# Performance work log

Measured on AMD Instinct MI355X. Metric: run time of the kernel, lower is better.

Reference implementation:

```python
import jax, jax.numpy as jnp
import numpy as np

B, S, D, H, DM = 2, 2048, 1024, 16, 4
HD = D // H  # head_dim = 64
EPS = 1e-5


def setup_inputs() -> dict:
    key = jax.random.key(0)
    ks = jax.random.split(key, 8)
    s = 0.02
    return {
        "x": jax.random.normal(ks[0], (B, S, D), jnp.float32),
        "wq": jax.random.normal(ks[1], (D, D), jnp.float32) * s,
        "wk": jax.random.normal(ks[2], (D, D), jnp.float32) * s,
        "wv": jax.random.normal(ks[3], (D, D), jnp.float32) * s,
        "wo": jax.random.normal(ks[4], (D, D), jnp.float32) * s,
        "bo": jnp.zeros((D,), jnp.float32),
        "ln1_scale": jnp.ones((D,), jnp.float32),
        "ln1_shift": jnp.zeros((D,), jnp.float32),
        "ln2_scale": jnp.ones((D,), jnp.float32),
        "ln2_shift": jnp.zeros((D,), jnp.float32),
        "w1": jax.random.normal(ks[5], (DM * D, D), jnp.float32) * s,
        "b1": jnp.zeros((DM * D,), jnp.float32),
        "w2": jax.random.normal(ks[6], (D, DM * D), jnp.float32) * s,
        "b2": jnp.zeros((D,), jnp.float32),
    }


def _layernorm(x, scale, shift):
    mean = jnp.mean(x, axis=-1, keepdims=True)
    var = jnp.var(x, axis=-1, keepdims=True)  # unbiased=False
    return scale * (x - mean) * jax.lax.rsqrt(var + EPS) + shift


def _attn(x, wq, wk, wv, wo, bo):
    b, n, d = x.shape
    # torch Linear: y = x @ W.T
    q = (x @ wq.T).reshape(b, n, H, HD).transpose(0, 2, 1, 3)  # [b,h,n,hd]
    k = (x @ wk.T).reshape(b, n, H, HD).transpose(0, 2, 1, 3)
    v = (x @ wv.T).reshape(b, n, H, HD).transpose(0, 2, 1, 3)
    scores = jnp.einsum("bhqd,bhkd->bhqk", q, k)
    causal = jnp.tril(jnp.ones((n, n), bool))
    scores = jnp.where(causal, scores, -jnp.inf)
    w = jax.nn.softmax(scores / np.sqrt(HD).astype(np.float32), axis=-1)
    ctx = jnp.einsum("bhqk,bhkd->bhqd", w, v)
    ctx = ctx.transpose(0, 2, 1, 3).reshape(b, n, d)
    return ctx @ wo.T + bo


def reference(x, wq, wk, wv, wo, bo, ln1_scale, ln1_shift, ln2_scale, ln2_shift, w1, b1, w2, b2):
    h = x + _attn(_layernorm(x, ln1_scale, ln1_shift), wq, wk, wv, wo, bo)
    y = _layernorm(h, ln2_scale, ln2_shift)
    y = jax.nn.relu(y @ w1.T + b1) @ w2.T + b2
    return h + y
```

## Files before the change

kernel.cpp:

```cpp
#include <hip/hip_runtime.h>
#include <hip/hip_bf16.h>

#define DEV __device__ __forceinline__

typedef __attribute__((ext_vector_type(8))) short bf8;
typedef __attribute__((ext_vector_type(4))) float f4;
typedef __attribute__((ext_vector_type(16))) float f16x;

#define GLOAD_LDS(gp, lp) \
  __builtin_amdgcn_global_load_lds( \
      (const __attribute__((address_space(1))) void*)(gp), \
      (__attribute__((address_space(3))) void*)(lp), 16, 0, 0)

DEV unsigned short f2bf(float f) {
  union { __hip_bfloat16 h; unsigned short u; } c;
  c.h = __float2bfloat16(f);
  return c.u;
}
DEV unsigned int pk2(float a, float b) {
  union { __hip_bfloat162 h; unsigned int u; } c;
  c.h = __hip_bfloat162(__float2bfloat16(a), __float2bfloat16(b));
  return c.u;
}

DEV int2 swz_tile(int ob, int nxt, int nyt) {
  const int nb = nxt * nyt;
  const int cpx = nb >> 3;
  const int W = (ob & 7) * cpx + (ob >> 3);
  const int scw = 4 * nyt;
  const int sc = W / scw, rem = W - sc * scw;
  return make_int2(rem >> 2, sc * 4 + (rem & 3));
}

template<bool BIAS, bool RELU, bool OUTBF, bool WRVT>
__global__ __launch_bounds__(512, 2) void gemm_bt256(
    const unsigned short* __restrict__ A, const unsigned short* __restrict__ B,
    const float* __restrict__ bias, void* __restrict__ Cout,
    int M, int N, int K, int ldc, unsigned short* __restrict__ vtout, int nyt)
{
  __shared__ unsigned short Sl[2][2][256 * 64];
  const int t = threadIdx.x;
  const int w = t >> 6, l = t & 63;
  const int wr = w >> 2, wc = w & 3;
  int2 tt = swz_tile((int)blockIdx.x, N >> 8, nyt);
  const int m0 = tt.x * 256, n0 = tt.y * 256;

  const int srow = w * 32 + (l >> 3);
  const int scol = 8 * ((l & 7) ^ (l >> 3));
  const unsigned short* Ab = A + (size_t)(m0 + srow) * K + scol;
  const unsigned short* Bb = B + (size_t)(n0 + srow) * K + scol;
  const int sdst = w * 2048 + l * 8;

  auto STAGE = [&](int slot, int kt) {
#pragma unroll
    for (int i = 0; i < 4; ++i) {
      GLOAD_LDS(Ab + (size_t)i * 8 * K + kt * 64, &Sl[slot][0][sdst + i * 512]);
      GLOAD_LDS(Bb + (size_t)i * 8 * K + kt * 64, &Sl[slot][1][sdst + i * 512]);
    }
  };

  const f4 fz = {0.f, 0.f, 0.f, 0.f};
  f4 acc[8][4];
#pragma unroll
  for (int i = 0; i < 8; ++i)
#pragma unroll
    for (int j = 0; j < 4; ++j) acc[i][j] = fz;

  const int NT = K >> 6;
  STAGE(0, 0);
  __syncthreads();

  for (int T = 0; T < NT; ++T) {
    if (T + 1 < NT) STAGE((T + 1) & 1, T + 1);
    const int sl = T & 1;
#pragma unroll
    for (int ks = 0; ks < 2; ++ks) {
      const int cb = (ks * 64 + ((l >> 4) * 16)) ^ ((l & 7) << 4);
      bf8 af[8], bg[4];
#pragma unroll
      for (int m = 0; m < 8; ++m)
        af[m] = *(const bf8*)((const char*)&Sl[sl][0][(wr * 128 + m * 16 + (l & 15)) * 64] + cb);
#pragma unroll
      for (int n = 0; n < 4; ++n)
        bg[n] = *(const bf8*)((const char*)&Sl[sl][1][(wc * 64 + n * 16 + (l & 15)) * 64] + cb);
      __builtin_amdgcn_s_setprio(1);
#pragma unroll
      for (int m = 0; m < 8; ++m)
#pragma unroll
        for (int n = 0; n < 4; ++n)
          acc[m][n] = __builtin_amdgcn_mfma_f32_16x16x32_bf16(af[m], bg[n], acc[m][n], 0, 0, 0);
      __builtin_amdgcn_s_setprio(0);
    }
    __syncthreads();
  }

#pragma unroll
  for (int n = 0; n < 4; ++n) {
    const int col = n0 + wc * 64 + n * 16 + (l & 15);
    float bv = 0.f;
    if (BIAS) bv = bias[col];
    const bool isv = WRVT && (col >= 2048);
    const int hh = (col - 2048) >> 6, dd = (col - 2048) & 63;
#pragma unroll
    for (int m = 0; m < 8; ++m) {
#pragma unroll
      for (int r = 0; r < 4; ++r) {
        const int row = m0 + wr * 128 + m * 16 + ((l >> 4) * 4) + r;
        float v = acc[m][n][r] + bv;
        if (RELU) v = fmaxf(v, 0.f);
        if (WRVT && isv) {
          const int bb = row >> 11, ss = row & 2047;
          vtout[((size_t)(bb * 16 + hh) * 64 + dd) * 2048 + ss] = f2bf(v);
        } else if (OUTBF) {
          ((unsigned short*)Cout)[(size_t)row * ldc + col] = f2bf(v);
        } else {
          ((float*)Cout)[(size_t)row * ldc + col] = v;
        }
      }
    }
  }
}

template<bool BIAS, bool RELU, bool RESID, bool OUTBF>
__global__ __launch_bounds__(256) void gemm_bt64(
    const unsigned short* __restrict__ A, const unsigned short* __restrict__ B,
    const float* __restrict__ bias, const float* __restrict__ resid,
    void* __restrict__ Cout, int M, int N, int K, int ldc)
{
  __shared__ unsigned short Al[2][64 * 64];
  __shared__ unsigned short Bl[2][128 * 64];
  const int t = threadIdx.x;
  const int w = t >> 6, l = t & 63;
  const int wr = w >> 1, wc = w & 1;
  int2 tt = swz_tile((int)blockIdx.x, N >> 7, M >> 6);
  const int m0 = tt.x * 64, n0 = tt.y * 128;

  const int srow = t >> 3;
  const int scol = 8 * ((t & 7) ^ (srow & 7));
  const unsigned short* Ab = A + (size_t)(m0 + srow) * K + scol;
  const unsigned short* Bb = B + (size_t)(n0 + srow) * K + scol;
  const int sdst = srow * 64 + (t & 7) * 8;

  auto STAGE = [&](int slot, int k0) {
#pragma unroll
    for (int i = 0; i < 2; ++i)
      GLOAD_LDS(Ab + (size_t)(i * 32) * K + k0, &Al[slot][sdst + i * 32 * 64]);
#pragma unroll
    for (int i = 0; i < 4; ++i)
      GLOAD_LDS(Bb + (size_t)(i * 32) * K + k0, &Bl[slot][sdst + i * 32 * 64]);
  };

  const f4 fz = {0.f, 0.f, 0.f, 0.f};
  f4 acc[2][4];
#pragma unroll
  for (int i = 0; i < 2; ++i)
#pragma unroll
    for (int j = 0; j < 4; ++j) acc[i][j] = fz;

  const int NT = K >> 6;
  STAGE(0, 0);
  __syncthreads();

  for (int T = 0; T < NT; ++T) {
    if (T + 1 < NT) STAGE((T + 1) & 1, (T + 1) * 64);
    const int sl = T & 1;
#pragma unroll
    for (int ks = 0; ks < 2; ++ks) {
      const int cb = (ks * 64 + ((l >> 4) * 16)) ^ ((l & 7) << 4);
      bf8 af[2], bg[4];
#pragma unroll
      for (int am = 0; am < 2; ++am)
        af[am] = *(const bf8*)((const char*)&Al[sl][(wr * 32 + am * 16 + (l & 15)) * 64] + cb);
#pragma unroll
      for (int bn = 0; bn < 4; ++bn)
        bg[bn] = *(const bf8*)((const char*)&Bl[sl][(wc * 64 + bn * 16 + (l & 15)) * 64] + cb);
      __builtin_amdgcn_s_setprio(1);
#pragma unroll
      for (int am = 0; am < 2; ++am)
#pragma unroll
        for (int bn = 0; bn < 4; ++bn)
          acc[am][bn] = __builtin_amdgcn_mfma_f32_16x16x32_bf16(af[am], bg[bn], acc[am][bn], 0, 0, 0);
      __builtin_amdgcn_s_setprio(0);
    }
    __syncthreads();
  }

#pragma unroll
  for (int bn = 0; bn < 4; ++bn) {
    const int col = n0 + wc * 64 + bn * 16 + (l & 15);
    float bv = 0.f;
    if (BIAS) bv = bias[col];
#pragma unroll
    for (int am = 0; am < 2; ++am) {
#pragma unroll
      for (int r = 0; r < 4; ++r) {
        const int row = m0 + wr * 32 + am * 16 + ((l >> 4) * 4) + r;
        float v = acc[am][bn][r] + bv;
        if (RELU) v = fmaxf(v, 0.f);
        if (RESID) v += resid[(size_t)row * ldc + col];
        if (OUTBF) ((unsigned short*)Cout)[(size_t)row * ldc + col] = f2bf(v);
        else       ((float*)Cout)[(size_t)row * ldc + col] = v;
      }
    }
  }
}

__global__ __launch_bounds__(256, 4) void attn_kernel(
    const unsigned short* __restrict__ qk, const unsigned short* __restrict__ vt,
    unsigned short* __restrict__ ctx)
{
  __shared__ unsigned short SM[2][2][64 * 64];

  const int t = threadIdx.x;
  const int w = t >> 6, l = t & 63;
  const int p = w >> 1;
  const int hi = l >> 5, q = l & 31;
  const int bid = blockIdx.x;
  const int xcd = bid & 7, i = bid >> 3;
  const int g = i >> 5, c = i & 31;
  const int s = (g & 1) ? c : 31 - c;
  const int bh = xcd * 4 + g;
  const int b = bh >> 4, h = bh & 15;
  const int tile = 2 * s + (w & 1);
  const int q0w = tile * 32;
  const int h0 = (s + 2) >> 1;

  const unsigned short* qbase = qk + ((size_t)b * 2048) * 2048 + h * 64;
  const unsigned short* kbase = qbase + 1024;
  const unsigned short* vbase = vt + (size_t)bh * 64 * 2048;
  unsigned short* Kl = &SM[p][0][0];
  unsigned short* Vl = &SM[p][1][0];
  const int tp = t & 127;

  bf8 qf[4];
#pragma unroll
  for (int ksl = 0; ksl < 4; ++ksl)
    qf[ksl] = *(const bf8*)(qbase + (size_t)(q0w + q) * 2048 + ksl * 16 + hi * 8);

  f16x oacc[2];
#pragma unroll
  for (int dn = 0; dn < 2; ++dn)
#pragma unroll
    for (int i2 = 0; i2 < 16; ++i2) oacc[dn][i2] = 0.f;
  float m_ = -1e30f, l_ = 0.f;

  for (int it = 0; it < h0; ++it) {
    const int gi = p ? h0 + it : it;
    const bool act = gi <= s;
    __syncthreads();
    if (act) {
#pragma unroll
      for (int ss = 0; ss < 4; ++ss) {
        const int row = ss * 16 + (tp >> 3);
        const int cb = (tp & 7) * 16;
        const int sb = cb ^ ((row & 7) << 4);
        GLOAD_LDS(kbase + (size_t)(gi * 64 + row) * 2048 + (sb >> 1),
                  &Kl[row * 64 + (cb >> 1)]);
        GLOAD_LDS(vbase + (size_t)row * 2048 + gi * 64 + (sb >> 1),
                  &Vl[row * 64 + (cb >> 1)]);
      }
    }
    __syncthreads();
    if (act) {
      const int kb0 = gi * 64;

      f16x s0, s1;
#pragma unroll
      for (int i2 = 0; i2 < 16; ++i2) { s0[i2] = 0.f; s1[i2] = 0.f; }
      __builtin_amdgcn_s_setprio(1);
#pragma unroll
      for (int ksl = 0; ksl < 4; ++ksl) {
        const int cbq = (ksl * 16 + hi * 8) * 2;
        const int r0 = q, r1 = 32 + q;
        bf8 k0 = *(const bf8*)((const char*)&Kl[r0 * 64] + (cbq ^ ((r0 & 7) << 4)));
        bf8 k1 = *(const bf8*)((const char*)&Kl[r1 * 64] + (cbq ^ ((r1 & 7) << 4)));
        s0 = __builtin_amdgcn_mfma_f32_32x32x16_bf16(k0, qf[ksl], s0, 0, 0, 0);
        s1 = __builtin_amdgcn_mfma_f32_32x32x16_bf16(k1, qf[ksl], s1, 0, 0, 0);
      }
      __builtin_amdgcn_s_setprio(0);

      float pv[32];
      if (gi == s) {
#pragma unroll
        for (int i2 = 0; i2 < 16; ++i2) {
          const int key = kb0 + (i2 & 3) + 8 * (i2 >> 2) + 4 * hi;
          pv[i2]      = (key <= q0w + q)      ? s0[i2] : -1e30f;
          pv[16 + i2] = (key + 32 <= q0w + q) ? s1[i2] : -1e30f;
        }
      } else {
#pragma unroll
        for (int i2 = 0; i2 < 16; ++i2) { pv[i2] = s0[i2]; pv[16 + i2] = s1[i2]; }
      }

      float tm[16];
#pragma unroll
      for (int i2 = 0; i2 < 16; ++i2) tm[i2] = fmaxf(pv[i2], pv[16 + i2]);
#pragma unroll
      for (int st = 8; st >= 1; st >>= 1)
#pragma unroll
        for (int i2 = 0; i2 < 8; ++i2)
          if (i2 < st) tm[i2] = fmaxf(tm[i2], tm[i2 + st]);
      const float pmax = fmaxf(tm[0], __shfl_xor(tm[0], 32));
      if (__any(pmax > m_ + 11.54f)) {
        const float mn = fmaxf(m_, pmax);
        const float alpha = __builtin_amdgcn_exp2f(m_ - mn);
        m_ = mn;
        l_ *= alpha;
#pragma unroll
        for (int dn = 0; dn < 2; ++dn)
#pragma unroll
          for (int i2 = 0; i2 < 16; ++i2) oacc[dn][i2] *= alpha;
      }
#pragma unroll
      for (int i2 = 0; i2 < 32; ++i2) pv[i2] = __builtin_amdgcn_exp2f(pv[i2] - m_);
      float ts[16];
#pragma unroll
      for (int i2 = 0; i2 < 16; ++i2) ts[i2] = pv[i2] + pv[16 + i2];
#pragma unroll
      for (int st = 8; st >= 1; st >>= 1)
#pragma unroll
        for (int i2 = 0; i2 < 8; ++i2)
          if (i2 < st) ts[i2] += ts[i2 + st];
      l_ += ts[0] + __shfl_xor(ts[0], 32);

#pragma unroll
      for (int sg = 0; sg < 2; ++sg) {
        const float* pp = pv + sg * 16;
        unsigned int wds[8];
#pragma unroll
        for (int m = 0; m < 4; ++m) {
          wds[m * 2]     = pk2(pp[4 * m], pp[4 * m + 1]);
          wds[m * 2 + 1] = pk2(pp[4 * m + 2], pp[4 * m + 3]);
        }
#pragma unroll
        for (int kq = 0; kq < 2; ++kq) {
          unsigned int x0 = __shfl_xor((int)(hi ? wds[4 * kq]     : wds[4 * kq + 2]), 32);
          unsigned int x1 = __shfl_xor((int)(hi ? wds[4 * kq + 1] : wds[4 * kq + 3]), 32);
          union { unsigned int u[4]; bf8 v; } pu;
          pu.u[0] = hi ? x0 : wds[4 * kq];
          pu.u[1] = hi ? x1 : wds[4 * kq + 1];
          pu.u[2] = hi ? wds[4 * kq + 2] : x0;
          pu.u[3] = hi ? wds[4 * kq + 3] : x1;
          const bf8 pf = pu.v;
          __builtin_amdgcn_s_setprio(1);
#pragma unroll
          for (int dn = 0; dn < 2; ++dn) {
            const int row = dn * 32 + q;
            const int cb = ((sg * 32 + kq * 16 + hi * 8) * 2) ^ ((row & 7) << 4);
            bf8 vf = *(const bf8*)((const char*)&Vl[row * 64] + cb);
            oacc[dn] = __builtin_amdgcn_mfma_f32_32x32x16_bf16(vf, pf, oacc[dn], 0, 0, 0);
          }
          __builtin_amdgcn_s_setprio(0);
        }
      }
    }
  }

  __syncthreads();
  float* mb = (float*)&SM[0][0][0];
  if (p == 1) {
    float* base = mb + (w & 1) * 2176;
    base[l] = m_;
    base[64 + l] = l_;
#pragma unroll
    for (int dn = 0; dn < 2; ++dn)
#pragma unroll
      for (int i2 = 0; i2 < 16; ++i2)
        base[128 + (dn * 16 + i2) * 64 + l] = oacc[dn][i2];
  }
  __syncthreads();
  if (p == 0) {
    float* base = mb + (w & 1) * 2176;
    const float m2 = base[l], l2 = base[64 + l];
    const float mm = fmaxf(m_, m2);
    const float a0 = __builtin_amdgcn_exp2f(m_ - mm);
    const float a2 = __builtin_amdgcn_exp2f(m2 - mm);
    const float inv = 1.0f / (a0 * l_ + a2 * l2);
    unsigned short* crow = ctx + ((size_t)(b * 2048 + q0w + q)) * 1024 + h * 64;
#pragma unroll
    for (int dn = 0; dn < 2; ++dn)
#pragma unroll
      for (int m = 0; m < 4; ++m) {
        float o0 = a0 * oacc[dn][4 * m]     + a2 * base[128 + (dn * 16 + 4 * m) * 64 + l];
        float o1 = a0 * oacc[dn][4 * m + 1] + a2 * base[128 + (dn * 16 + 4 * m + 1) * 64 + l];
        float o2 = a0 * oacc[dn][4 * m + 2] + a2 * base[128 + (dn * 16 + 4 * m + 2) * 64 + l];
        float o3 = a0 * oacc[dn][4 * m + 3] + a2 * base[128 + (dn * 16 + 4 * m + 3) * 64 + l];
        const int d0 = dn * 32 + 8 * m + 4 * hi;
        *(unsigned int*)(crow + d0)     = pk2(o0 * inv, o1 * inv);
        *(unsigned int*)(crow + d0 + 2) = pk2(o2 * inv, o3 * inv);
      }
  }
}

__global__ __launch_bounds__(256) void ln_kernel(
    const float* __restrict__ x, const float* __restrict__ sc,
    const float* __restrict__ sh, unsigned short* __restrict__ out)
{
  const int row = blockIdx.x, t = threadIdx.x;
  float4 v = ((const float4*)x)[(size_t)row * 256 + t];
  float s = v.x + v.y + v.z + v.w;
  float q = v.x * v.x + v.y * v.y + v.z * v.z + v.w * v.w;
#pragma unroll
  for (int off = 1; off < 64; off <<= 1) {
    s += __shfl_xor(s, off);
    q += __shfl_xor(q, off);
  }
  __shared__ float red[8];
  const int w = t >> 6, l = t & 63;
  if (l == 0) { red[w] = s; red[4 + w] = q; }
  __syncthreads();
  s = red[0] + red[1] + red[2] + red[3];
  q = red[4] + red[5] + red[6] + red[7];
  const float mean = s * (1.0f / 1024.0f);
  const float var = q * (1.0f / 1024.0f) - mean * mean;
  const float rstd = rsqrtf(var + 1e-5f);
  float4 scv = ((const float4*)sc)[t];
  float4 shv = ((const float4*)sh)[t];
  uint2 p;
  p.x = pk2(scv.x * (v.x - mean) * rstd + shv.x, scv.y * (v.y - mean) * rstd + shv.y);
  p.y = pk2(scv.z * (v.z - mean) * rstd + shv.z, scv.w * (v.w - mean) * rstd + shv.w);
  ((uint2*)out)[(size_t)row * 256 + t] = p;
}

__global__ __launch_bounds__(256) void cvt_weights(
    const float* __restrict__ wq, const float* __restrict__ wk,
    const float* __restrict__ wv, const float* __restrict__ wo,
    const float* __restrict__ w1, const float* __restrict__ w2,
    unsigned short* __restrict__ dst)
{
  const int M1 = 1 << 20;
  const int n4 = (12 * M1) / 4;
  const int stride = gridDim.x * 256;
  for (int i4 = blockIdx.x * 256 + threadIdx.x; i4 < n4; i4 += stride) {
    const size_t i = (size_t)i4 * 4;
    const int mi = (int)(i >> 20);
    const float* src;
    size_t off;
    float sc = 1.0f;
    if (mi < 4) {
      src = mi == 0 ? wq : mi == 1 ? wk : mi == 2 ? wv : wo;
      off = i & (size_t)(M1 - 1);
      if (mi == 0) sc = 0.125f * 1.44269504088896f;
    } else if (mi < 8) {
      src = w1; off = i - (size_t)4 * M1;
    } else {
      src = w2; off = i - (size_t)8 * M1;
    }
    float4 v = *(const float4*)(src + off);
    uint2 pq;
    pq.x = pk2(v.x * sc, v.y * sc);
    pq.y = pk2(v.z * sc, v.w * sc);
    ((uint2*)dst)[i4] = pq;
  }
}

extern "C" void kernel_launch(void* const* d_in, const int* in_sizes, int n_in,
                              void* d_out, int out_size, void* d_ws, size_t ws_size,
                              hipStream_t stream)
{
  const float* x    = (const float*)d_in[0];
  const float* wq   = (const float*)d_in[1];
  const float* wk   = (const float*)d_in[2];
  const float* wv   = (const float*)d_in[3];
  const float* wo   = (const float*)d_in[4];
  const float* bo   = (const float*)d_in[5];
  const float* ln1s = (const float*)d_in[6];
  const float* ln1b = (const float*)d_in[7];
  const float* ln2s = (const float*)d_in[8];
  const float* ln2b = (const float*)d_in[9];
  const float* w1   = (const float*)d_in[10];
  const float* b1   = (const float*)d_in[11];
  const float* w2   = (const float*)d_in[12];
  const float* b2   = (const float*)d_in[13];
  float* out = (float*)d_out;

  const int M = 4096;

  unsigned short* ws   = (unsigned short*)d_ws;
  unsigned short* lnb  = ws;
  unsigned short* qkvw = lnb  + (size_t)4096 * 1024;
  unsigned short* wob  = qkvw + (size_t)3072 * 1024;
  unsigned short* w1b  = wob  + (size_t)1024 * 1024;
  unsigned short* w2b  = w1b  + (size_t)4096 * 1024;
  unsigned short* qkb  = w2b  + (size_t)4096 * 1024;
  unsigned short* vtb  = qkb  + (size_t)4096 * 2048;
  unsigned short* ctxb = vtb  + (size_t)32 * 64 * 2048;
  float* hf = (float*)(ctxb + (size_t)4096 * 1024);

  cvt_weights<<<2048, 256, 0, stream>>>(wq, wk, wv, wo, w1, w2, qkvw);

  ln_kernel<<<M, 256, 0, stream>>>(x, ln1s, ln1b, lnb);
  gemm_bt256<false, false, true, true><<<192, 512, 0, stream>>>(
      lnb, qkvw, nullptr, qkb, M, 3072, 1024, 2048, vtb, 16);
  attn_kernel<<<1024, 256, 0, stream>>>(qkb, vtb, ctxb);
  gemm_bt64<true, false, true, false><<<512, 256, 0, stream>>>(
      ctxb, wob, bo, x, hf, M, 1024, 1024, 1024);
  ln_kernel<<<M, 256, 0, stream>>>(hf, ln2s, ln2b, lnb);
  gemm_bt256<true, true, true, false><<<256, 512, 0, stream>>>(
      lnb, w1b, b1, qkb, M, 4096, 1024, 4096, nullptr, 16);
  gemm_bt64<true, false, true, false><<<512, 256, 0, stream>>>(
      qkb, w2b, b2, hf, out, M, 1024, 4096, 1024);
}
```

Baseline: 237.2 us.

## Replace 256x256 GEMM kernel with 128x128 tiles, BK=32, 256 threads

Replaces the 512-thread 256x256-tile GEMM with a 256-thread 128x128-tile variant that uses BK=32, a new LDS swizzle and a smaller accumulator set. It also adds an optional residual epilogue. The QKV and FFN1 launches move to 768 and 1024 blocks. This trades per-block data reuse and MFMA density for more blocks, better CU occupancy and less LDS per block, at the cost of more global traffic and more barriers per unit of work.

```diff
diff --git a/kernel.cpp b/kernel.cpp
--- a/kernel.cpp
+++ b/kernel.cpp
@@ -32,82 +32,82 @@
   return make_int2(rem >> 2, sc * 4 + (rem & 3));
 }
 
-template<bool BIAS, bool RELU, bool OUTBF, bool WRVT>
-__global__ __launch_bounds__(512, 2) void gemm_bt256(
+template<bool BIAS, bool RELU, bool RESID, bool OUTBF, bool WRVT>
+__global__ __launch_bounds__(256) void gemm_bt128(
     const unsigned short* __restrict__ A, const unsigned short* __restrict__ B,
-    const float* __restrict__ bias, void* __restrict__ Cout,
-    int M, int N, int K, int ldc, unsigned short* __restrict__ vtout, int nyt)
+    const float* __restrict__ bias, const float* __restrict__ resid,
+    void* __restrict__ Cout, int M, int N, int K, int ldc,
+    unsigned short* __restrict__ vtout, int nyt)
 {
-  __shared__ unsigned short Sl[2][2][256 * 64];
+  __shared__ unsigned short Al[2][128 * 32];
+  __shared__ unsigned short Bl[2][128 * 32];
   const int t = threadIdx.x;
   const int w = t >> 6, l = t & 63;
-  const int wr = w >> 2, wc = w & 3;
-  int2 tt = swz_tile((int)blockIdx.x, N >> 8, nyt);
-  const int m0 = tt.x * 256, n0 = tt.y * 256;
-
-  const int srow = w * 32 + (l >> 3);
-  const int scol = 8 * ((l & 7) ^ (l >> 3));
-  const unsigned short* Ab = A + (size_t)(m0 + srow) * K + scol;
-  const unsigned short* Bb = B + (size_t)(n0 + srow) * K + scol;
-  const int sdst = w * 2048 + l * 8;
-
-  auto STAGE = [&](int slot, int kt) {
-#pragma unroll
-    for (int i = 0; i < 4; ++i) {
-      GLOAD_LDS(Ab + (size_t)i * 8 * K + kt * 64, &Sl[slot][0][sdst + i * 512]);
-      GLOAD_LDS(Bb + (size_t)i * 8 * K + kt * 64, &Sl[slot][1][sdst + i * 512]);
+  const int wr = w >> 1, wc = w & 1;
+  int2 tt = swz_tile((int)blockIdx.x, N >> 7, nyt);
+  const int m0 = tt.x * 128, n0 = tt.y * 128;
+
+  const int srow = w * 16 + (l >> 2);
+  const int scsw = ((l & 3) * 8) ^ (((srow >> 1) & 3) << 3);
+  const unsigned short* Ab = A + (size_t)(m0 + srow) * K + scsw;
+  const unsigned short* Bb = B + (size_t)(n0 + srow) * K + scsw;
+  const int sdst = w * 512 + l * 8;
+
+  auto STAGE = [&](int slot, int k0) {
+#pragma unroll
+    for (int i = 0; i < 2; ++i) {
+      GLOAD_LDS(Ab + (size_t)i * 64 * K + k0, &Al[slot][sdst + i * 2048]);
+      GLOAD_LDS(Bb + (size_t)i * 64 * K + k0, &Bl[slot][sdst + i * 2048]);
     }
   };
 
   const f4 fz = {0.f, 0.f, 0.f, 0.f};
-  f4 acc[8][4];
-#pragma unroll
-  for (int i = 0; i < 8; ++i)
+  f4 acc[4][4];
+#pragma unroll
+  for (int i = 0; i < 4; ++i)
 #pragma unroll
     for (int j = 0; j < 4; ++j) acc[i][j] = fz;
 
-  const int NT = K >> 6;
+  const int NT = K >> 5;
   STAGE(0, 0);
   __syncthreads();
 
   for (int T = 0; T < NT; ++T) {
-    if (T + 1 < NT) STAGE((T + 1) & 1, T + 1);
+    if (T + 1 < NT) STAGE((T + 1) & 1, (T + 1) * 32);
     const int sl = T & 1;
-#pragma unroll
-    for (int ks = 0; ks < 2; ++ks) {
-      const int cb = (ks * 64 + ((l >> 4) * 16)) ^ ((l & 7) << 4);
-      bf8 af[8], bg[4];
-#pragma unroll
-      for (int m = 0; m < 8; ++m)
-        af[m] = *(const bf8*)((const char*)&Sl[sl][0][(wr * 128 + m * 16 + (l & 15)) * 64] + cb);
-#pragma unroll
-      for (int n = 0; n < 4; ++n)
-        bg[n] = *(const bf8*)((const char*)&Sl[sl][1][(wc * 64 + n * 16 + (l & 15)) * 64] + cb);
-      __builtin_amdgcn_s_setprio(1);
-#pragma unroll
-      for (int m = 0; m < 8; ++m)
-#pragma unroll
-        for (int n = 0; n < 4; ++n)
-          acc[m][n] = __builtin_amdgcn_mfma_f32_16x16x32_bf16(af[m], bg[n], acc[m][n], 0, 0, 0);
-      __builtin_amdgcn_s_setprio(0);
-    }
+    const int rdcol = ((l >> 4) * 8) ^ ((((l & 15) >> 1) & 3) << 3);
+    bf8 af[4], bg[4];
+#pragma unroll
+    for (int am = 0; am < 4; ++am)
+      af[am] = *(const bf8*)&Al[sl][(wr * 64 + am * 16 + (l & 15)) * 32 + rdcol];
+#pragma unroll
+    for (int bn = 0; bn < 4; ++bn)
+      bg[bn] = *(const bf8*)&Bl[sl][(wc * 64 + bn * 16 + (l & 15)) * 32 + rdcol];
+    __builtin_amdgcn_s_setprio(1);
+#pragma unroll
+    for (int am = 0; am < 4; ++am)
+#pragma unroll
+      for (int bn = 0; bn < 4; ++bn)
+        acc[am][bn] = __builtin_amdgcn_mfma_f32_16x16x32_bf16(af[am], bg[bn], acc[am][bn], 0, 0, 0);
+    __builtin_amdgcn_s_setprio(0);
     __syncthreads();
   }
 
 #pragma unroll
-  for (int n = 0; n < 4; ++n) {
-    const int col = n0 + wc * 64 + n * 16 + (l & 15);
+  for (int bn = 0; bn < 4; ++bn) {
+    const int col = n0 + wc * 64 + bn * 16 + (l & 15);
     float bv = 0.f;
     if (BIAS) bv = bias[col];
     const bool isv = WRVT && (col >= 2048);
     const int hh = (col - 2048) >> 6, dd = (col - 2048) & 63;
 #pragma unroll
-    for (int m = 0; m < 8; ++m) {
+    for (int am = 0; am < 4; ++am) {
 #pragma unroll
       for (int r = 0; r < 4; ++r) {
-        const int row = m0 + wr * 128 + m * 16 + ((l >> 4) * 4) + r;
-        float v = acc[m][n][r] + bv;
+        const int row = m0 + wr * 64 + am * 16 + ((l >> 4) * 4) + r;
+        float v = acc[am][bn][r] + bv;
         if (RELU) v = fmaxf(v, 0.f);
+        if (RESID) v += resid[(size_t)row * ldc + col];
         if (WRVT && isv) {
           const int bb = row >> 11, ss = row & 2047;
           vtout[((size_t)(bb * 16 + hh) * 64 + dd) * 2048 + ss] = f2bf(v);
@@ -490,14 +490,14 @@
   cvt_weights<<<2048, 256, 0, stream>>>(wq, wk, wv, wo, w1, w2, qkvw);
 
   ln_kernel<<<M, 256, 0, stream>>>(x, ln1s, ln1b, lnb);
-  gemm_bt256<false, false, true, true><<<192, 512, 0, stream>>>(
-      lnb, qkvw, nullptr, qkb, M, 3072, 1024, 2048, vtb, 16);
+  gemm_bt128<false, false, false, true, true><<<768, 256, 0, stream>>>(
+      lnb, qkvw, nullptr, nullptr, qkb, M, 3072, 1024, 2048, vtb, 32);
   attn_kernel<<<1024, 256, 0, stream>>>(qkb, vtb, ctxb);
   gemm_bt64<true, false, true, false><<<512, 256, 0, stream>>>(
       ctxb, wob, bo, x, hf, M, 1024, 1024, 1024);
   ln_kernel<<<M, 256, 0, stream>>>(hf, ln2s, ln2b, lnb);
-  gemm_bt256<true, true, true, false><<<256, 512, 0, stream>>>(
-      lnb, w1b, b1, qkb, M, 4096, 1024, 4096, nullptr, 16);
+  gemm_bt128<true, true, false, true, false><<<1024, 256, 0, stream>>>(
+      lnb, w1b, b1, nullptr, qkb, M, 4096, 1024, 4096, nullptr, 32);
   gemm_bt64<true, false, true, false><<<512, 256, 0, stream>>>(
       qkb, w2b, b2, hf, out, M, 1024, 4096, 1024);
 }
```

Result: no change. 236.2 us (-0.4%).
